# Performance work log

Hardware: AMD Instinct MI355X
Metric: run time of the kernel (lower is better)

## Reference

```python
import jax, jax.numpy as jnp
import numpy as np


def setup_inputs() -> dict:
    key = jax.random.key(0)
    k1, k2 = jax.random.split(key)
    B, P, C, N = 32, 3, 512, 1024
    input_data1 = jax.random.normal(k1, (B, P, C, N), dtype=jnp.float32)
    input_data2 = jax.random.normal(k2, (B, P, C, N), dtype=jnp.float32)
    return {"input_data1": input_data1, "input_data2": input_data2}


def reference(input_data1, input_data2):
    # HorizontalComparisonModel.compare_algorithm_method4 (the only path used):
    # permute [B,P,C,N] -> [B,P,N,C], reshape to [B, P*N, C] pairs of C-dim vectors.
    B = input_data1.shape[0]
    x = jnp.transpose(input_data1, (0, 1, 3, 2)).reshape(B, -1, input_data1.shape[2])
    y = jnp.transpose(input_data2, (0, 1, 3, 2)).reshape(B, -1, input_data2.shape[2])
    d = x - y                                   # [B, pairs, C]
    l1 = jnp.sum(jnp.abs(d), axis=-1)           # temp31: L1 distance
    sq_l2 = jnp.sum(d * d, axis=-1)             # temp21: squared L2 distance
    # Original stacks [temp31, temp21, temp31] (L1 appears twice; cosine unused).
    out = jnp.stack([l1, sq_l2, l1], axis=-1)   # [B, pairs, 3]
    return out.reshape(B, -1)
```

## Files before the change

kernel.cpp:

```cpp
#include <hip/hip_runtime.h>

constexpr int B = 32, P = 3, C = 512, N = 1024;
constexpr int G = B * P;
constexpr int CSPLIT = 16;
constexpr int CCHUNK = C / CSPLIT;
constexpr size_t WS_NEED = (size_t)CSPLIT * G * N * 2 * sizeof(float);

__global__ __launch_bounds__(256) void dist_partial(
    const float* __restrict__ x1, const float* __restrict__ x2,
    float* __restrict__ ws)
{
    const int g     = blockIdx.x / CSPLIT;
    const int chunk = blockIdx.x % CSPLIT;
    const int t     = threadIdx.x;

    const float4* pa = (const float4*)(x1 + (size_t)g * C * N)
                       + (size_t)chunk * CCHUNK * (N / 4) + t;
    const float4* pb = (const float4*)(x2 + (size_t)g * C * N)
                       + (size_t)chunk * CCHUNK * (N / 4) + t;

    float4 l1 = make_float4(0.f, 0.f, 0.f, 0.f);
    float4 l2 = make_float4(0.f, 0.f, 0.f, 0.f);

    #pragma unroll
    for (int j = 0; j < CCHUNK; j += 4) {
        const float4 a0 = pa[0 * (N / 4)];
        const float4 a1 = pa[1 * (N / 4)];
        const float4 a2 = pa[2 * (N / 4)];
        const float4 a3 = pa[3 * (N / 4)];
        const float4 b0 = pb[0 * (N / 4)];
        const float4 b1 = pb[1 * (N / 4)];
        const float4 b2 = pb[2 * (N / 4)];
        const float4 b3 = pb[3 * (N / 4)];
        pa += N;
        pb += N;
        float d;
        d = a0.x - b0.x; l1.x += fabsf(d); l2.x = fmaf(d, d, l2.x);
        d = a0.y - b0.y; l1.y += fabsf(d); l2.y = fmaf(d, d, l2.y);
        d = a0.z - b0.z; l1.z += fabsf(d); l2.z = fmaf(d, d, l2.z);
        d = a0.w - b0.w; l1.w += fabsf(d); l2.w = fmaf(d, d, l2.w);
        d = a1.x - b1.x; l1.x += fabsf(d); l2.x = fmaf(d, d, l2.x);
        d = a1.y - b1.y; l1.y += fabsf(d); l2.y = fmaf(d, d, l2.y);
        d = a1.z - b1.z; l1.z += fabsf(d); l2.z = fmaf(d, d, l2.z);
        d = a1.w - b1.w; l1.w += fabsf(d); l2.w = fmaf(d, d, l2.w);
        d = a2.x - b2.x; l1.x += fabsf(d); l2.x = fmaf(d, d, l2.x);
        d = a2.y - b2.y; l1.y += fabsf(d); l2.y = fmaf(d, d, l2.y);
        d = a2.z - b2.z; l1.z += fabsf(d); l2.z = fmaf(d, d, l2.z);
        d = a2.w - b2.w; l1.w += fabsf(d); l2.w = fmaf(d, d, l2.w);
        d = a3.x - b3.x; l1.x += fabsf(d); l2.x = fmaf(d, d, l2.x);
        d = a3.y - b3.y; l1.y += fabsf(d); l2.y = fmaf(d, d, l2.y);
        d = a3.z - b3.z; l1.z += fabsf(d); l2.z = fmaf(d, d, l2.z);
        d = a3.w - b3.w; l1.w += fabsf(d); l2.w = fmaf(d, d, l2.w);
    }

    float4* wout = (float4*)ws + ((size_t)(chunk * G + g) * N) / 2 + 2 * t;
    wout[0] = make_float4(l1.x, l2.x, l1.y, l2.y);
    wout[1] = make_float4(l1.z, l2.z, l1.w, l2.w);
}

__global__ __launch_bounds__(256) void dist_combine(
    const float* __restrict__ ws, float* __restrict__ out)
{
    const int idx = blockIdx.x * 256 + threadIdx.x;
    const float2* ws2 = (const float2*)ws;
    float l1 = 0.f, l2 = 0.f;
    #pragma unroll
    for (int chunk = 0; chunk < CSPLIT; ++chunk) {
        const float2 v = ws2[(size_t)chunk * G * N + idx];
        l1 += v.x;
        l2 += v.y;
    }
    out[3 * (size_t)idx + 0] = l1;
    out[3 * (size_t)idx + 1] = l2;
    out[3 * (size_t)idx + 2] = l1;
}

__global__ __launch_bounds__(256) void dist_atomic(
    const float* __restrict__ x1, const float* __restrict__ x2,
    float* __restrict__ out)
{
    const int g     = blockIdx.x / CSPLIT;
    const int chunk = blockIdx.x % CSPLIT;
    const int t     = threadIdx.x;
    const float4* a = (const float4*)(x1 + (size_t)g * C * N) + t;
    const float4* b = (const float4*)(x2 + (size_t)g * C * N) + t;
    const int c0 = chunk * CCHUNK;
    float4 l1 = make_float4(0.f, 0.f, 0.f, 0.f);
    float4 l2 = make_float4(0.f, 0.f, 0.f, 0.f);
    for (int c = c0; c < c0 + CCHUNK; ++c) {
        const float4 av = a[(size_t)c * (N / 4)];
        const float4 bv = b[(size_t)c * (N / 4)];
        float d;
        d = av.x - bv.x; l1.x += fabsf(d); l2.x = fmaf(d, d, l2.x);
        d = av.y - bv.y; l1.y += fabsf(d); l2.y = fmaf(d, d, l2.y);
        d = av.z - bv.z; l1.z += fabsf(d); l2.z = fmaf(d, d, l2.z);
        d = av.w - bv.w; l1.w += fabsf(d); l2.w = fmaf(d, d, l2.w);
    }
    const size_t obase = ((size_t)g * N + 4 * (size_t)t) * 3;
    const float l1v[4] = {l1.x, l1.y, l1.z, l1.w};
    const float l2v[4] = {l2.x, l2.y, l2.z, l2.w};
    #pragma unroll
    for (int i = 0; i < 4; ++i) {
        atomicAdd(&out[obase + 3 * i + 0], l1v[i]);
        atomicAdd(&out[obase + 3 * i + 1], l2v[i]);
        atomicAdd(&out[obase + 3 * i + 2], l1v[i]);
    }
}

extern "C" void kernel_launch(void* const* d_in, const int* in_sizes, int n_in,
                              void* d_out, int out_size, void* d_ws, size_t ws_size,
                              hipStream_t stream) {
    const float* x1 = (const float*)d_in[0];
    const float* x2 = (const float*)d_in[1];
    float* out = (float*)d_out;

    if (ws_size >= WS_NEED) {
        dist_partial<<<G * CSPLIT, 256, 0, stream>>>(x1, x2, (float*)d_ws);
        dist_combine<<<(G * N) / 256, 256, 0, stream>>>((const float*)d_ws, out);
    } else {
        hipMemsetAsync(d_out, 0, (size_t)out_size * sizeof(float), stream);
        dist_atomic<<<G * CSPLIT, 256, 0, stream>>>(x1, x2, out);
    }
}
```

Baseline: 392.6 us.

## Interleave channel rows across split blocks and add 32-way split path

Each block now reads channel rows strided by the split count (chunk, chunk+CS, ...) instead of a contiguous chunk of rows, which changes how concurrent blocks spread their DRAM accesses. A templated 32-way channel split is added and used when the workspace is large enough, doubling the number of blocks for more parallelism. The cost is a larger workspace write and a combine pass that reads twice as many partials.

```diff
diff --git a/kernel.cpp b/kernel.cpp
--- a/kernel.cpp
+++ b/kernel.cpp
@@ -2,38 +2,36 @@
 
 constexpr int B = 32, P = 3, C = 512, N = 1024;
 constexpr int G = B * P;
-constexpr int CSPLIT = 16;
-constexpr int CCHUNK = C / CSPLIT;
-constexpr size_t WS_NEED = (size_t)CSPLIT * G * N * 2 * sizeof(float);
 
+template <int CS>
 __global__ __launch_bounds__(256) void dist_partial(
     const float* __restrict__ x1, const float* __restrict__ x2,
     float* __restrict__ ws)
 {
-    const int g     = blockIdx.x / CSPLIT;
-    const int chunk = blockIdx.x % CSPLIT;
+    constexpr int ROWS = C / CS;
+    const int g     = blockIdx.x / CS;
+    const int chunk = blockIdx.x % CS;
     const int t     = threadIdx.x;
 
     const float4* pa = (const float4*)(x1 + (size_t)g * C * N)
-                       + (size_t)chunk * CCHUNK * (N / 4) + t;
+                       + (size_t)chunk * (N / 4) + t;
     const float4* pb = (const float4*)(x2 + (size_t)g * C * N)
-                       + (size_t)chunk * CCHUNK * (N / 4) + t;
+                       + (size_t)chunk * (N / 4) + t;
+    constexpr size_t RSTRIDE = (size_t)CS * (N / 4);
 
     float4 l1 = make_float4(0.f, 0.f, 0.f, 0.f);
     float4 l2 = make_float4(0.f, 0.f, 0.f, 0.f);
 
     #pragma unroll
-    for (int j = 0; j < CCHUNK; j += 4) {
-        const float4 a0 = pa[0 * (N / 4)];
-        const float4 a1 = pa[1 * (N / 4)];
-        const float4 a2 = pa[2 * (N / 4)];
-        const float4 a3 = pa[3 * (N / 4)];
-        const float4 b0 = pb[0 * (N / 4)];
-        const float4 b1 = pb[1 * (N / 4)];
-        const float4 b2 = pb[2 * (N / 4)];
-        const float4 b3 = pb[3 * (N / 4)];
-        pa += N;
-        pb += N;
+    for (int j = 0; j < ROWS; j += 4) {
+        const float4 a0 = pa[(j + 0) * RSTRIDE];
+        const float4 a1 = pa[(j + 1) * RSTRIDE];
+        const float4 a2 = pa[(j + 2) * RSTRIDE];
+        const float4 a3 = pa[(j + 3) * RSTRIDE];
+        const float4 b0 = pb[(j + 0) * RSTRIDE];
+        const float4 b1 = pb[(j + 1) * RSTRIDE];
+        const float4 b2 = pb[(j + 2) * RSTRIDE];
+        const float4 b3 = pb[(j + 3) * RSTRIDE];
         float d;
         d = a0.x - b0.x; l1.x += fabsf(d); l2.x = fmaf(d, d, l2.x);
         d = a0.y - b0.y; l1.y += fabsf(d); l2.y = fmaf(d, d, l2.y);
@@ -58,6 +56,7 @@
     wout[1] = make_float4(l1.z, l2.z, l1.w, l2.w);
 }
 
+template <int CS>
 __global__ __launch_bounds__(256) void dist_combine(
     const float* __restrict__ ws, float* __restrict__ out)
 {
@@ -65,7 +64,7 @@
     const float2* ws2 = (const float2*)ws;
     float l1 = 0.f, l2 = 0.f;
     #pragma unroll
-    for (int chunk = 0; chunk < CSPLIT; ++chunk) {
+    for (int chunk = 0; chunk < CS; ++chunk) {
         const float2 v = ws2[(size_t)chunk * G * N + idx];
         l1 += v.x;
         l2 += v.y;
@@ -79,15 +78,16 @@
     const float* __restrict__ x1, const float* __restrict__ x2,
     float* __restrict__ out)
 {
-    const int g     = blockIdx.x / CSPLIT;
-    const int chunk = blockIdx.x % CSPLIT;
+    constexpr int CS = 16;
+    const int g     = blockIdx.x / CS;
+    const int chunk = blockIdx.x % CS;
     const int t     = threadIdx.x;
     const float4* a = (const float4*)(x1 + (size_t)g * C * N) + t;
     const float4* b = (const float4*)(x2 + (size_t)g * C * N) + t;
-    const int c0 = chunk * CCHUNK;
     float4 l1 = make_float4(0.f, 0.f, 0.f, 0.f);
     float4 l2 = make_float4(0.f, 0.f, 0.f, 0.f);
-    for (int c = c0; c < c0 + CCHUNK; ++c) {
+    for (int j = 0; j < C / CS; ++j) {
+        const int c = chunk + CS * j;
         const float4 av = a[(size_t)c * (N / 4)];
         const float4 bv = b[(size_t)c * (N / 4)];
         float d;
@@ -114,11 +114,17 @@
     const float* x2 = (const float*)d_in[1];
     float* out = (float*)d_out;
 
-    if (ws_size >= WS_NEED) {
-        dist_partial<<<G * CSPLIT, 256, 0, stream>>>(x1, x2, (float*)d_ws);
-        dist_combine<<<(G * N) / 256, 256, 0, stream>>>((const float*)d_ws, out);
+    const size_t need32 = (size_t)32 * G * N * 2 * sizeof(float);
+    const size_t need16 = (size_t)16 * G * N * 2 * sizeof(float);
+
+    if (ws_size >= need32) {
+        dist_partial<32><<<G * 32, 256, 0, stream>>>(x1, x2, (float*)d_ws);
+        dist_combine<32><<<(G * N) / 256, 256, 0, stream>>>((const float*)d_ws, out);
+    } else if (ws_size >= need16) {
+        dist_partial<16><<<G * 16, 256, 0, stream>>>(x1, x2, (float*)d_ws);
+        dist_combine<16><<<(G * N) / 256, 256, 0, stream>>>((const float*)d_ws, out);
     } else {
         hipMemsetAsync(d_out, 0, (size_t)out_size * sizeof(float), stream);
-        dist_atomic<<<G * CSPLIT, 256, 0, stream>>>(x1, x2, out);
+        dist_atomic<<<G * 16, 256, 0, stream>>>(x1, x2, out);
     }
 }
```

Result: no change. 393.9 us (+0.4%).
